# Performance work log

Hardware: AMD Instinct MI355X
Metric: run time of the kernel (lower is better)

The kernel has to match this reference:

```python
import jax, jax.numpy as jnp
import numpy as np

OUT_FEATURES = 12288
IN_FEATURES = 8192
GROUP_SIZE = 64
N_GROUPS = IN_FEATURES // GROUP_SIZE      # 128
N_GROUP_IDS = GROUP_SIZE // 4             # 16 packed uint16 words per group
BATCH, SEQ = 4, 128


def _dequant(w_packed, w_scale, w_bias):
    """Unpack int4 nibbles and rescale: faithful to group_quantize_decompress.

    Packing layout (from _int4_npy_encoder): over the flattened quantized
    tensor, blocks of 16 values map to 4 packed words; value at position
    4*i + j within a block is nibble i of packed word j. The original
    decoder's float16 bit tricks ((bits & 0xF) viewed as fp16 * 2^24, etc.)
    are exactly nibble extraction.
    """
    R, G, I = w_packed.shape
    p = w_packed.reshape(R, G, I // 4, 4)                 # (R, G, blk, j)
    nibs = jnp.stack([(p >> (4 * i)) & 0xF for i in range(4)], axis=-2)  # (R, G, blk, i, j)
    unpacked = nibs.reshape(R, G, I * 4).astype(w_scale.dtype)
    w = unpacked * w_scale + w_bias                        # group scale/bias broadcast
    return w.reshape(R, G * I * 4)                         # (out_features, in_features)


def setup_inputs() -> dict:
    key = jax.random.key(0)
    k1, k2, k3, k4 = jax.random.split(key, 4)
    x = jax.random.normal(k1, (BATCH, SEQ, IN_FEATURES), dtype=jnp.float32)
    w_packed = jax.random.randint(k2, (OUT_FEATURES, N_GROUPS, N_GROUP_IDS), 0, 65536, dtype=jnp.int32)
    w_scale = jax.random.uniform(k3, (OUT_FEATURES, N_GROUPS, 1), dtype=jnp.float32) * 0.1
    w_bias = jax.random.normal(k4, (OUT_FEATURES, N_GROUPS, 1), dtype=jnp.float32) * 0.05
    return {"x": x, "w_packed": w_packed, "w_scale": w_scale, "w_bias": w_bias}


def reference(x, w_packed, w_scale, w_bias):
    weight = _dequant(w_packed, w_scale, w_bias)           # (O, I)
    return jnp.einsum('bsi,oi->bso', x, weight)            # F.linear, bias=None
```

## Files before the change

### kernel.cpp

```cpp
#include <hip/hip_runtime.h>
#include <hip/hip_bf16.h>

#define OUTF 12288
#define INF  8192
#define NGRP 128
#define MTOT 512

#define BM 128
#define BN 128
#define BK 64
#define NKT (INF / BK)

typedef _Float16 h2 __attribute__((ext_vector_type(2)));
typedef _Float16 h8 __attribute__((ext_vector_type(8)));
typedef float    f4 __attribute__((ext_vector_type(4)));

union U2 { unsigned int u; h2 h; };

__global__ __launch_bounds__(256) void xconvert(const float* __restrict__ x,
                                                _Float16* __restrict__ xh)
{
    int t = blockIdx.x * 256 + threadIdx.x;
    const float4* src = (const float4*)(x + (size_t)t * 16);
    float4 a = src[0];
    float4 b = src[1];
    float4 c = src[2];
    float4 d = src[3];
    U2 o0, o1, o2, o3, o4, o5, o6, o7;
    o0.h = h2{(_Float16)a.x, (_Float16)c.x};
    o1.h = h2{(_Float16)a.y, (_Float16)c.y};
    o2.h = h2{(_Float16)a.z, (_Float16)c.z};
    o3.h = h2{(_Float16)a.w, (_Float16)c.w};
    o4.h = h2{(_Float16)b.x, (_Float16)d.x};
    o5.h = h2{(_Float16)b.y, (_Float16)d.y};
    o6.h = h2{(_Float16)b.z, (_Float16)d.z};
    o7.h = h2{(_Float16)b.w, (_Float16)d.w};
    uint4* dst = (uint4*)(xh + (size_t)t * 16);
    dst[0] = make_uint4(o0.u, o1.u, o2.u, o3.u);
    dst[1] = make_uint4(o4.u, o5.u, o6.u, o7.u);
}

__global__ __launch_bounds__(256, 2) void gql_mfma(
    const _Float16* __restrict__ xh,
    const int*      __restrict__ wp,
    const float*    __restrict__ wsc,
    const float*    __restrict__ wbi,
    float*          __restrict__ out)
{
    __shared__ __align__(16) unsigned char ldsA[2][BM * BK * 2];
    __shared__ __align__(16) unsigned char ldsB[2][BN * BK * 2];

    const int tid  = threadIdx.x;
    const int lane = tid & 63;
    const int wv   = tid >> 6;
    const int wr   = wv >> 1;
    const int wc   = wv & 1;

    const int bm = blockIdx.x & 3;
    const int bn = blockIdx.x >> 2;
    const int m0 = bm * BM;
    const int n0 = bn * BN;

    const _Float16* asrc[4];
#pragma unroll
    for (int ia = 0; ia < 4; ++ia) {
        int L    = ia * 4096 + tid * 16;
        int row  = L >> 7;
        int ksw  = L & 127;
        int ksrc = ksw ^ ((row & 7) << 4);
        asrc[ia] = xh + (size_t)(m0 + row) * INF + (ksrc >> 1);
    }

    const int olb = tid >> 2;
    const int blk = tid & 3;
    size_t wpo[2]; int sbo[2]; int bw0[2];
#pragma unroll
    for (int it = 0; it < 2; ++it) {
        int ol  = it * 64 + olb;
        wpo[it] = (size_t)(n0 + ol) * NGRP * 16 + blk * 4;
        sbo[it] = (n0 + ol) * NGRP;
        bw0[it] = ol * 128 + ((blk * 32) ^ ((ol & 7) << 4));
    }

    f4 acc[4][4];
#pragma unroll
    for (int i = 0; i < 4; ++i)
#pragma unroll
        for (int j = 0; j < 4; ++j)
            acc[i][j] = f4{0.f, 0.f, 0.f, 0.f};

    uint4 wreg[2]; float sreg[2], breg[2];

    auto loadB = [&](int kt) {
#pragma unroll
        for (int it = 0; it < 2; ++it) {
            wreg[it] = *(const uint4*)(wp + wpo[it] + (size_t)kt * 16);
            sreg[it] = wsc[sbo[it] + kt];
            breg[it] = wbi[sbo[it] + kt];
        }
    };

    auto stageA = [&](int kt, int bufsel) {
#pragma unroll
        for (int ia = 0; ia < 4; ++ia) {
            __builtin_amdgcn_global_load_lds(
                (const __attribute__((address_space(1))) void*)(asrc[ia] + kt * 64),
                (__attribute__((address_space(3))) void*)(&ldsA[bufsel][ia * 4096 + tid * 16]),
                16, 0, 0);
        }
    };

    auto dequant = [&](int bufsel) {
#pragma unroll
        for (int it = 0; it < 2; ++it) {
            _Float16 sh = (_Float16)(sreg[it] * 4096.0f);
            _Float16 bh = (_Float16)breg[it];
            h2 S  = h2{sh, sh};
            h2 Bv = h2{bh, bh};
            h2 K  = h2{(_Float16)4096.0f, (_Float16)4096.0f};
            unsigned int wa[4] = {wreg[it].x, wreg[it].y, wreg[it].z, wreg[it].w};
            unsigned int ow[8];
#pragma unroll
            for (int j = 0; j < 4; ++j) {
                unsigned int w  = wa[j];
                unsigned int t2 = w | (w << 8);
                U2 c02, c13, r02, r13;
                c02.u = t2 & 0x000F000Fu;
                c13.u = (t2 >> 4) & 0x000F000Fu;
                r02.h = (c02.h * K) * S + Bv;
                r13.h = (c13.h * K) * S + Bv;
                ow[j]     = r02.u;
                ow[4 + j] = r13.u;
            }
            *(uint4*)(&ldsB[bufsel][bw0[it]])      = make_uint4(ow[0], ow[1], ow[2], ow[3]);
            *(uint4*)(&ldsB[bufsel][bw0[it] ^ 16]) = make_uint4(ow[4], ow[5], ow[6], ow[7]);
        }
    };

    auto compute = [&](int bufsel) {
#pragma unroll
        for (int kk = 0; kk < 2; ++kk) {
            h8 af[4], bf[4];
#pragma unroll
            for (int i = 0; i < 4; ++i) {
                int row = wr * 64 + i * 16 + (lane & 15);
                int off = row * 128 + ((kk * 64 + ((lane >> 4) << 4)) ^ ((row & 7) << 4));
                af[i] = *(const h8*)(&ldsA[bufsel][off]);
            }
#pragma unroll
            for (int j = 0; j < 4; ++j) {
                int col = wc * 64 + j * 16 + (lane & 15);
                int off = col * 128 + ((kk * 64 + ((lane >> 4) << 4)) ^ ((col & 7) << 4));
                bf[j] = *(const h8*)(&ldsB[bufsel][off]);
            }
#pragma unroll
            for (int i = 0; i < 4; ++i)
#pragma unroll
                for (int j = 0; j < 4; ++j)
                    acc[i][j] = __builtin_amdgcn_mfma_f32_16x16x32_f16(af[i], bf[j], acc[i][j], 0, 0, 0);
        }
    };

    loadB(0);
    stageA(0, 0);
    dequant(0);
    __syncthreads();

    for (int kt = 0; kt < NKT; ++kt) {
        int cur = kt & 1;
        if (kt + 1 < NKT) {
            loadB(kt + 1);
            stageA(kt + 1, cur ^ 1);
        }
        compute(cur);
        if (kt + 1 < NKT) dequant(cur ^ 1);
        __syncthreads();
    }

    const int cr = (lane >> 4) << 2;
    const int cc = lane & 15;
#pragma unroll
    for (int i = 0; i < 4; ++i)
#pragma unroll
        for (int j = 0; j < 4; ++j) {
            int grow = m0 + wr * 64 + i * 16 + cr;
            int gcol = n0 + wc * 64 + j * 16 + cc;
            float* p = out + (size_t)grow * OUTF + gcol;
            p[0 * OUTF] = acc[i][j][0];
            p[1 * OUTF] = acc[i][j][1];
            p[2 * OUTF] = acc[i][j][2];
            p[3 * OUTF] = acc[i][j][3];
        }
}

extern "C" void kernel_launch(void* const* d_in, const int* in_sizes, int n_in,
                              void* d_out, int out_size, void* d_ws, size_t ws_size,
                              hipStream_t stream)
{
    const float* x  = (const float*)d_in[0];
    const int*   wq = (const int*)d_in[1];
    const float* ws = (const float*)d_in[2];
    const float* wb = (const float*)d_in[3];
    float* o        = (float*)d_out;
    _Float16* xh    = (_Float16*)d_ws;

    xconvert<<<(MTOT * (size_t)INF / 16) / 256, 256, 0, stream>>>(x, xh);
    gql_mfma<<<(MTOT / BM) * (OUTF / BN), 256, 0, stream>>>(xh, wq, ws, wb, o);
}
```

Measured before the change: 373.9 us.

## Halve N tile, swizzle blocks, and pipeline loads with explicit vmcnt barriers

Reduces the N tile to 64 columns with launch bounds allowing three blocks per CU, remaps block indices so neighbouring blocks share weight rows, and unrolls the main loop by two with double-buffered weight prefetch registers. It replaces __syncthreads with a partial s_waitcnt vmcnt barrier so the next weight loads stay in flight across the barrier, and precomputes the LDS fragment offsets. The aim is better latency hiding and wave balance across CUs. In exchange, activation tiles are fetched twice as often per output and the kernel relies on exact count bookkeeping of outstanding loads.

```diff
diff --git a/kernel.cpp b/kernel.cpp
--- a/kernel.cpp
+++ b/kernel.cpp
@@ -3,13 +3,12 @@
 
 #define OUTF 12288
 #define INF  8192
-#define NGRP 128
 #define MTOT 512
 
 #define BM 128
-#define BN 128
+#define BN 64
 #define BK 64
-#define NKT (INF / BK)
+#define NKT 128
 
 typedef _Float16 h2 __attribute__((ext_vector_type(2)));
 typedef _Float16 h8 __attribute__((ext_vector_type(8)));
@@ -40,7 +39,7 @@
     dst[1] = make_uint4(o4.u, o5.u, o6.u, o7.u);
 }
 
-__global__ __launch_bounds__(256, 2) void gql_mfma(
+__global__ __launch_bounds__(256, 3) void gql_mfma(
     const _Float16* __restrict__ xh,
     const int*      __restrict__ wp,
     const float*    __restrict__ wsc,
@@ -56,141 +55,148 @@
     const int wr   = wv >> 1;
     const int wc   = wv & 1;
 
-    const int bm = blockIdx.x & 3;
-    const int bn = blockIdx.x >> 2;
-    const int m0 = bm * BM;
-    const int n0 = bn * BN;
+    const int swz = (blockIdx.x & 7) * 96 + (blockIdx.x >> 3);
+    const int m0  = (swz & 3) * BM;
+    const int n0  = (swz >> 2) * BN;
 
     const _Float16* asrc[4];
 #pragma unroll
     for (int ia = 0; ia < 4; ++ia) {
         int L    = ia * 4096 + tid * 16;
         int row  = L >> 7;
-        int ksw  = L & 127;
-        int ksrc = ksw ^ ((row & 7) << 4);
+        int ksrc = (L & 127) ^ ((row & 7) << 4);
         asrc[ia] = xh + (size_t)(m0 + row) * INF + (ksrc >> 1);
     }
 
-    const int olb = tid >> 2;
-    const int blk = tid & 3;
-    size_t wpo[2]; int sbo[2]; int bw0[2];
-#pragma unroll
-    for (int it = 0; it < 2; ++it) {
-        int ol  = it * 64 + olb;
-        wpo[it] = (size_t)(n0 + ol) * NGRP * 16 + blk * 4;
-        sbo[it] = (n0 + ol) * NGRP;
-        bw0[it] = ol * 128 + ((blk * 32) ^ ((ol & 7) << 4));
+    const int brow = tid >> 2;
+    const int bblk = tid & 3;
+    const size_t wpo = (size_t)(n0 + brow) * 2048 + bblk * 4;
+    const int sco = (n0 + brow) * 128;
+    const int bw0 = brow * 128 + ((bblk * 32) ^ ((brow & 7) << 4));
+
+    int aoff[2][4], boff[2][2];
+#pragma unroll
+    for (int kk = 0; kk < 2; ++kk) {
+        int kb = kk * 64 + ((lane >> 4) << 4);
+#pragma unroll
+        for (int i = 0; i < 4; ++i) {
+            int row = wr * 64 + i * 16 + (lane & 15);
+            aoff[kk][i] = row * 128 + (kb ^ ((row & 7) << 4));
+        }
+#pragma unroll
+        for (int j = 0; j < 2; ++j) {
+            int col = wc * 32 + j * 16 + (lane & 15);
+            boff[kk][j] = col * 128 + (kb ^ ((col & 7) << 4));
+        }
     }
 
-    f4 acc[4][4];
+    f4 acc[4][2];
 #pragma unroll
     for (int i = 0; i < 4; ++i)
 #pragma unroll
-        for (int j = 0; j < 4; ++j)
+        for (int j = 0; j < 2; ++j)
             acc[i][j] = f4{0.f, 0.f, 0.f, 0.f};
 
-    uint4 wreg[2]; float sreg[2], breg[2];
-
-    auto loadB = [&](int kt) {
-#pragma unroll
-        for (int it = 0; it < 2; ++it) {
-            wreg[it] = *(const uint4*)(wp + wpo[it] + (size_t)kt * 16);
-            sreg[it] = wsc[sbo[it] + kt];
-            breg[it] = wbi[sbo[it] + kt];
-        }
-    };
-
-    auto stageA = [&](int kt, int bufsel) {
-#pragma unroll
-        for (int ia = 0; ia < 4; ++ia) {
+    uint4 w0, w1; float s0, s1, b0, b1;
+
+    auto stageA = [&](int kt, int buf) {
+#pragma unroll
+        for (int ia = 0; ia < 4; ++ia)
             __builtin_amdgcn_global_load_lds(
                 (const __attribute__((address_space(1))) void*)(asrc[ia] + kt * 64),
-                (__attribute__((address_space(3))) void*)(&ldsA[bufsel][ia * 4096 + tid * 16]),
+                (__attribute__((address_space(3))) void*)(&ldsA[buf][ia * 4096 + tid * 16]),
                 16, 0, 0);
-        }
-    };
-
-    auto dequant = [&](int bufsel) {
-#pragma unroll
-        for (int it = 0; it < 2; ++it) {
-            _Float16 sh = (_Float16)(sreg[it] * 4096.0f);
-            _Float16 bh = (_Float16)breg[it];
-            h2 S  = h2{sh, sh};
-            h2 Bv = h2{bh, bh};
-            h2 K  = h2{(_Float16)4096.0f, (_Float16)4096.0f};
-            unsigned int wa[4] = {wreg[it].x, wreg[it].y, wreg[it].z, wreg[it].w};
-            unsigned int ow[8];
-#pragma unroll
-            for (int j = 0; j < 4; ++j) {
-                unsigned int w  = wa[j];
-                unsigned int t2 = w | (w << 8);
-                U2 c02, c13, r02, r13;
-                c02.u = t2 & 0x000F000Fu;
-                c13.u = (t2 >> 4) & 0x000F000Fu;
-                r02.h = (c02.h * K) * S + Bv;
-                r13.h = (c13.h * K) * S + Bv;
-                ow[j]     = r02.u;
-                ow[4 + j] = r13.u;
-            }
-            *(uint4*)(&ldsB[bufsel][bw0[it]])      = make_uint4(ow[0], ow[1], ow[2], ow[3]);
-            *(uint4*)(&ldsB[bufsel][bw0[it] ^ 16]) = make_uint4(ow[4], ow[5], ow[6], ow[7]);
-        }
-    };
-
-    auto compute = [&](int bufsel) {
+        __builtin_amdgcn_sched_barrier(0);
+    };
+
+    auto loadB = [&](int kt, uint4& w, float& s, float& b) {
+        w = *(const uint4*)(wp + wpo + (size_t)kt * 16);
+        s = wsc[sco + kt];
+        b = wbi[sco + kt];
+    };
+
+    auto dequant = [&](uint4 w, float s, float b, int buf) {
+        _Float16 sh = (_Float16)(s * 4096.0f);
+        _Float16 bh = (_Float16)b;
+        h2 S  = h2{sh, sh};
+        h2 Bv = h2{bh, bh};
+        h2 K  = h2{(_Float16)4096.0f, (_Float16)4096.0f};
+        unsigned int wa[4] = {w.x, w.y, w.z, w.w};
+        unsigned int ow[8];
+#pragma unroll
+        for (int j = 0; j < 4; ++j) {
+            unsigned int t2 = wa[j] | (wa[j] << 8);
+            U2 c02, c13, r02, r13;
+            c02.u = t2 & 0x000F000Fu;
+            c13.u = (t2 >> 4) & 0x000F000Fu;
+            r02.h = (c02.h * K) * S + Bv;
+            r13.h = (c13.h * K) * S + Bv;
+            ow[j]     = r02.u;
+            ow[4 + j] = r13.u;
+        }
+        *(uint4*)(&ldsB[buf][bw0])      = make_uint4(ow[0], ow[1], ow[2], ow[3]);
+        *(uint4*)(&ldsB[buf][bw0 ^ 16]) = make_uint4(ow[4], ow[5], ow[6], ow[7]);
+    };
+
+    auto compute = [&](int buf) {
 #pragma unroll
         for (int kk = 0; kk < 2; ++kk) {
-            h8 af[4], bf[4];
-#pragma unroll
-            for (int i = 0; i < 4; ++i) {
-                int row = wr * 64 + i * 16 + (lane & 15);
-                int off = row * 128 + ((kk * 64 + ((lane >> 4) << 4)) ^ ((row & 7) << 4));
-                af[i] = *(const h8*)(&ldsA[bufsel][off]);
-            }
-#pragma unroll
-            for (int j = 0; j < 4; ++j) {
-                int col = wc * 64 + j * 16 + (lane & 15);
-                int off = col * 128 + ((kk * 64 + ((lane >> 4) << 4)) ^ ((col & 7) << 4));
-                bf[j] = *(const h8*)(&ldsB[bufsel][off]);
-            }
+            h8 af[4], bf[2];
+#pragma unroll
+            for (int i = 0; i < 4; ++i) af[i] = *(const h8*)(&ldsA[buf][aoff[kk][i]]);
+#pragma unroll
+            for (int j = 0; j < 2; ++j) bf[j] = *(const h8*)(&ldsB[buf][boff[kk][j]]);
 #pragma unroll
             for (int i = 0; i < 4; ++i)
 #pragma unroll
-                for (int j = 0; j < 4; ++j)
+                for (int j = 0; j < 2; ++j)
                     acc[i][j] = __builtin_amdgcn_mfma_f32_16x16x32_f16(af[i], bf[j], acc[i][j], 0, 0, 0);
         }
     };
 
-    loadB(0);
+#define KBAR(n) do { asm volatile("s_waitcnt vmcnt(" #n ") lgkmcnt(0)" ::: "memory"); \
+                     __builtin_amdgcn_s_barrier(); } while (0)
+
     stageA(0, 0);
-    dequant(0);
-    __syncthreads();
-
-    for (int kt = 0; kt < NKT; ++kt) {
-        int cur = kt & 1;
-        if (kt + 1 < NKT) {
-            loadB(kt + 1);
-            stageA(kt + 1, cur ^ 1);
-        }
-        compute(cur);
-        if (kt + 1 < NKT) dequant(cur ^ 1);
-        __syncthreads();
+    loadB(0, w0, s0, b0);
+    loadB(1, w1, s1, b1);
+    dequant(w0, s0, b0, 0);
+    KBAR(3);
+
+    for (int kt = 0; kt < NKT - 2; kt += 2) {
+        stageA(kt + 1, 1);
+        loadB(kt + 2, w0, s0, b0);
+        compute(0);
+        dequant(w1, s1, b1, 1);
+        KBAR(3);
+
+        stageA(kt + 2, 0);
+        loadB(kt + 3, w1, s1, b1);
+        compute(1);
+        dequant(w0, s0, b0, 0);
+        KBAR(3);
     }
+    stageA(NKT - 1, 1);
+    compute(0);
+    dequant(w1, s1, b1, 1);
+    KBAR(0);
+    compute(1);
 
     const int cr = (lane >> 4) << 2;
     const int cc = lane & 15;
 #pragma unroll
     for (int i = 0; i < 4; ++i)
 #pragma unroll
-        for (int j = 0; j < 4; ++j) {
+        for (int j = 0; j < 2; ++j) {
             int grow = m0 + wr * 64 + i * 16 + cr;
-            int gcol = n0 + wc * 64 + j * 16 + cc;
+            int gcol = n0 + wc * 32 + j * 16 + cc;
             float* p = out + (size_t)grow * OUTF + gcol;
             p[0 * OUTF] = acc[i][j][0];
             p[1 * OUTF] = acc[i][j][1];
             p[2 * OUTF] = acc[i][j][2];
             p[3 * OUTF] = acc[i][j][3];
         }
+#undef KBAR
 }
 
 extern "C" void kernel_launch(void* const* d_in, const int* in_sizes, int n_in,
```

Measured after the change: 312.2 us. -16.5%, faster.
